# Kernel tuning notes

Hardware: AMD Instinct MI355X
Metric: run time of the kernel (lower is better)

The kernel has to match this reference:

```python
import jax, jax.numpy as jnp
import numpy as np

# dims
N = 50000      # total nodes in merged batch graph
M = 250000     # edges for GNN propagation
E = 200000     # candidate edges scored by mixture-Bernoulli head
MAXN = 512     # max_num_nodes (padded adjacency row length)
H = 128        # hidden_dim = embedding_dim = msg_dim
EF = 128       # edge_feat_dim = 2 * att_edge_dim
ATT = 128      # att_hidden_dim
K = 20         # num_mix_component
L = 3          # num_GNN_layers
S = 512        # num_subgraph
B = 16         # batch of graphs
C = 1          # num_canonical_order


def setup_inputs() -> dict:
    key = jax.random.key(0)
    ks = list(jax.random.split(key, 64))
    it = iter(ks)
    nk = lambda: next(it)
    d = {}
    d['node_feat'] = jax.random.normal(nk(), (N, MAXN), jnp.float32)
    d['edge'] = jax.random.randint(nk(), (M, 2), 0, N, dtype=jnp.int32)
    d['edge_feat'] = jax.random.normal(nk(), (M, EF), jnp.float32)
    d['node_idx_gnn'] = jax.random.randint(nk(), (E, 2), 0, N, dtype=jnp.int32)
    d['label'] = (jax.random.uniform(nk(), (E,)) < 0.1).astype(jnp.float32)
    # even sorted partition of E candidate edges into S subgraphs (all nonempty)
    d['subgraph_idx'] = ((jnp.arange(E) * S) // E).astype(jnp.int32)
    # bc_idx = repeat_interleave(arange(B*C), subgraphs_per_graph)
    d['bc_idx'] = jnp.repeat(jnp.arange(B * C, dtype=jnp.int32), S // (B * C))
    # params
    def lin(k, out_d, in_d):
        return jax.random.normal(k, (out_d, in_d), jnp.float32) * (1.0 / np.sqrt(in_d))
    d['dec_W'] = lin(nk(), H, MAXN); d['dec_b'] = jnp.zeros((H,), jnp.float32)
    d['msg_W1'] = jnp.stack([lin(nk(), H, H + EF) for _ in range(L)])
    d['msg_b1'] = jnp.zeros((L, H), jnp.float32)
    d['msg_W2'] = jnp.stack([lin(nk(), H, H) for _ in range(L)])
    d['msg_b2'] = jnp.zeros((L, H), jnp.float32)
    d['att_W1'] = jnp.stack([lin(nk(), ATT, H + EF) for _ in range(L)])
    d['att_b1'] = jnp.zeros((L, ATT), jnp.float32)
    d['att_W2'] = jnp.stack([lin(nk(), H, ATT) for _ in range(L)])
    d['att_b2'] = jnp.zeros((L, H), jnp.float32)
    d['gru_Wih'] = jnp.stack([lin(nk(), 3 * H, H) for _ in range(L)])
    d['gru_bih'] = jnp.zeros((L, 3 * H), jnp.float32)
    d['gru_Whh'] = jnp.stack([lin(nk(), 3 * H, H) for _ in range(L)])
    d['gru_bhh'] = jnp.zeros((L, 3 * H), jnp.float32)
    d['th_W1'] = lin(nk(), H, H); d['th_b1'] = jnp.zeros((H,), jnp.float32)
    d['th_W2'] = lin(nk(), H, H); d['th_b2'] = jnp.zeros((H,), jnp.float32)
    d['th_W3'] = lin(nk(), K, H); d['th_b3'] = jnp.zeros((K,), jnp.float32)
    d['al_W1'] = lin(nk(), H, H); d['al_b1'] = jnp.zeros((H,), jnp.float32)
    d['al_W2'] = lin(nk(), H, H); d['al_b2'] = jnp.zeros((H,), jnp.float32)
    d['al_W3'] = lin(nk(), K, H); d['al_b3'] = jnp.zeros((K,), jnp.float32)
    return d


def _gran_forward(node_feat, edge_feat, label, dec_W, dec_b, msg_W1, msg_b1,
                  msg_W2, msg_b2, att_W1, att_b1, att_W2, att_b2, gru_Wih,
                  gru_bih, gru_Whh, gru_bhh, th_W1, th_b1, th_W2, th_b2,
                  th_W3, th_b3, al_W1, al_b1, al_W2, al_b2, al_W3, al_b3,
                  edge, node_idx_gnn, subgraph_idx, bc_idx):
    n = node_feat.shape[0]
    # decoder_input: Linear(max_num_nodes -> embedding_dim)
    state = node_feat @ dec_W.T + dec_b  # [N, H]
    src, dst = edge[:, 0], edge[:, 1]
    for l in range(L):
        if l > 0:
            state = jax.nn.relu(state)
        # _prop: gather diff, msg MLP, sigmoid attention gate, scatter-sum, GRU
        diff = state[src] - state[dst]                       # [M, H]
        ei = jnp.concatenate([diff, edge_feat], axis=1)      # [M, H+EF]
        msg = jax.nn.relu(ei @ msg_W1[l].T + msg_b1[l]) @ msg_W2[l].T + msg_b2[l]
        att = jax.nn.sigmoid(jax.nn.relu(ei @ att_W1[l].T + att_b1[l]) @ att_W2[l].T + att_b2[l])
        agg = jax.ops.segment_sum(msg * att, dst, num_segments=n)  # [N, H]
        # torch GRUCell
        gi = agg @ gru_Wih[l].T + gru_bih[l]
        gh = state @ gru_Whh[l].T + gru_bhh[l]
        i_r, i_z, i_n = jnp.split(gi, 3, axis=-1)
        h_r, h_z, h_n = jnp.split(gh, 3, axis=-1)
        r = jax.nn.sigmoid(i_r + h_r)
        z = jax.nn.sigmoid(i_z + h_z)
        nn_ = jnp.tanh(i_n + r * h_n)
        state = (1.0 - z) * nn_ + z * state
    # mixture-Bernoulli heads on candidate-edge node-state diffs
    d2 = state[node_idx_gnn[:, 0]] - state[node_idx_gnn[:, 1]]  # [E, H]
    def mlp3(x, W1, b1, W2, b2, W3, b3):
        h = jax.nn.relu(x @ W1.T + b1)
        h = jax.nn.relu(h @ W2.T + b2)
        return h @ W3.T + b3
    log_theta = mlp3(d2, th_W1, th_b1, th_W2, th_b2, th_W3, th_b3)  # [E, K]
    log_alpha = mlp3(d2, al_W1, al_b1, al_W2, al_b2, al_W3, al_b3)  # [E, K]
    # mixture_bernoulli_loss (pos_weight = 1.0)
    y = label[:, None]
    adj_loss = jax.nn.softplus(-log_theta) + (1.0 - y) * log_theta  # BCEWithLogits, [E, K]
    const = jax.ops.segment_sum(jnp.ones((label.shape[0],), log_theta.dtype), subgraph_idx, num_segments=S)
    reduce_adj = jax.ops.segment_sum(adj_loss, subgraph_idx, num_segments=S)     # [S, K]
    reduce_la = jax.ops.segment_sum(log_alpha, subgraph_idx, num_segments=S)
    reduce_la = jax.nn.log_softmax(reduce_la / const[:, None], axis=-1)
    log_prob = jax.scipy.special.logsumexp(-reduce_adj + reduce_la, axis=1)      # [S]
    bc_log_prob = jax.ops.segment_sum(log_prob, bc_idx, num_segments=B * C)
    bc_const = jax.ops.segment_sum(const, bc_idx, num_segments=B * C)
    bc_loss = (bc_log_prob / bc_const).reshape(B, C)
    b_loss = jax.scipy.special.logsumexp(bc_loss, axis=1)  # logsumexp over orderings
    return jnp.mean(-b_loss)


def reference(node_feat, edge, edge_feat, node_idx_gnn, label, subgraph_idx,
              bc_idx, dec_W, dec_b, msg_W1, msg_b1, msg_W2, msg_b2, att_W1,
              att_b1, att_W2, att_b2, gru_Wih, gru_bih, gru_Whh, gru_bhh,
              th_W1, th_b1, th_W2, th_b2, th_W3, th_b3, al_W1, al_b1, al_W2,
              al_b2, al_W3, al_b3):
    return _gran_forward(node_feat, edge_feat, label, dec_W, dec_b, msg_W1,
                         msg_b1, msg_W2, msg_b2, att_W1, att_b1, att_W2,
                         att_b2, gru_Wih, gru_bih, gru_Whh, gru_bhh, th_W1,
                         th_b1, th_W2, th_b2, th_W3, th_b3, al_W1, al_b1,
                         al_W2, al_b2, al_W3, al_b3, edge, node_idx_gnn,
                         subgraph_idx, bc_idx)
```

## Files before the change

kernel.cpp:

```cpp
#include <hip/hip_runtime.h>
#include <cstdint>
#include <cstddef>


typedef __bf16 bf16x8 __attribute__((ext_vector_type(8)));
typedef short  s16x8  __attribute__((ext_vector_type(8)));
typedef short  s16x4  __attribute__((ext_vector_type(4)));
typedef float  f32x4  __attribute__((ext_vector_type(4)));

__device__ inline unsigned short f2bf(float f) {
    return __builtin_bit_cast(unsigned short, (__bf16)f);
}
__device__ inline float bf2f(unsigned short b) {
    return __uint_as_float(((unsigned int)b) << 16);
}
__device__ inline unsigned int pk2(float a, float b) {
    return ((unsigned int)f2bf(b) << 16) | f2bf(a);
}
__device__ inline f32x4 MFMA(bf16x8 a, bf16x8 b, f32x4 c) {
    return __builtin_amdgcn_mfma_f32_16x16x32_bf16(a, b, c, 0, 0, 0);
}

__device__ inline bf16x8 ld_swz(const char* lds, int row, int unit) {
    return *(const bf16x8*)(lds + row * 256 + ((unit ^ (row & 7)) << 4));
}
__device__ inline void hid_write(char* HID, int h0, int erow, s16x4 s4) {
    int unit = h0 >> 3;
    *(s16x4*)(HID + erow * 256 + ((unit ^ (erow & 7)) << 4) + ((h0 & 4) << 1)) = s4;
}
__device__ inline s16x4 ld_swz4(const char* lds, int row, int c0) {
    int unit = c0 >> 3;
    return *(const s16x4*)(lds + row * 256 + ((unit ^ (row & 7)) << 4) + ((c0 & 4) << 1));
}
__device__ inline bf16x8 ldA(const short* __restrict__ Wb, int K, int row, int koff) {
    return *(const bf16x8*)(Wb + (size_t)row * K + koff);
}
__device__ inline bf16x8 ld_f32_frag(const float* __restrict__ p) {
    float4 a = *(const float4*)p, b = *(const float4*)(p + 4);
    s16x8 s;
    s[0] = f2bf(a.x); s[1] = f2bf(a.y); s[2] = f2bf(a.z); s[3] = f2bf(a.w);
    s[4] = f2bf(b.x); s[5] = f2bf(b.y); s[6] = f2bf(b.z); s[7] = f2bf(b.w);
    return __builtin_bit_cast(bf16x8, s);
}

#define NPACK 31
struct PrepackArgs {
    const float* src[NPACK];
    short*       dst[NPACK];
    int stride[NPACK];
    int rows[NPACK];
    int rowsTot[NPACK];
    int cols[NPACK];
};

__global__ void prepack(PrepackArgs a) {
    int e = blockIdx.y;
    int row = blockIdx.x;
    if (row >= a.rowsTot[e]) return;
    int c8 = threadIdx.x;
    if (c8 * 8 >= a.cols[e]) return;
    s16x8 s = {};
    if (row < a.rows[e]) {
        const float* p = a.src[e] + (size_t)row * a.stride[e] + c8 * 8;
        float4 x = *(const float4*)p, y = *(const float4*)(p + 4);
        s[0] = f2bf(x.x); s[1] = f2bf(x.y); s[2] = f2bf(x.z); s[3] = f2bf(x.w);
        s[4] = f2bf(y.x); s[5] = f2bf(y.y); s[6] = f2bf(y.z); s[7] = f2bf(y.w);
    }
    *(s16x8*)(a.dst[e] + (size_t)row * a.cols[e] + c8 * 8) = s;
}

__device__ inline void proj_gemm_store(const char* ST, char* PJ,
                                       const short* __restrict__ projW,
                                       short* __restrict__ proj,
                                       int rb, int R, int tid)
{
    const int l = tid & 63, w = tid >> 6;
    f32x4 accP[2][2][4] = {};
#pragma unroll
    for (int ks = 0; ks < 4; ++ks) {
        int koff = ks * 32 + (l >> 4) * 8;
        bf16x8 aw[2][2];
#pragma unroll
        for (int pc = 0; pc < 2; ++pc)
#pragma unroll
            for (int mt = 0; mt < 2; ++mt)
                aw[pc][mt] = ldA(projW, 128, pc * 128 + 32 * w + 16 * mt + (l & 15), koff);
#pragma unroll
        for (int n = 0; n < 4; ++n) {
            bf16x8 b = ld_swz(ST, 16 * n + (l & 15), ks * 4 + (l >> 4));
#pragma unroll
            for (int pc = 0; pc < 2; ++pc)
#pragma unroll
                for (int mt = 0; mt < 2; ++mt)
                    accP[pc][mt][n] = MFMA(aw[pc][mt], b, accP[pc][mt][n]);
        }
    }
    const int half = w >> 1;
#pragma unroll
    for (int hh = 0; hh < 2; ++hh) {
        __syncthreads();
        if (half == hh) {
#pragma unroll
            for (int pc = 0; pc < 2; ++pc)
#pragma unroll
                for (int mt = 0; mt < 2; ++mt) {
                    int h0 = 32 * w + 16 * mt + ((l >> 4) << 2);
                    int colp = 2 * h0 + 4 * pc - 128 * hh;
#pragma unroll
                    for (int n = 0; n < 4; ++n) {
                        f32x4 v = accP[pc][mt][n];
                        s16x4 s4;
                        s4[0] = f2bf(v[0]); s4[1] = f2bf(v[1]);
                        s4[2] = f2bf(v[2]); s4[3] = f2bf(v[3]);
                        hid_write(PJ, colp, 16 * n + (l & 15), s4);
                    }
                }
        }
        __syncthreads();
#pragma unroll
        for (int p2 = 0; p2 < 4; ++p2) {
            int row = p2 * 16 + (tid >> 4);
            int r = rb + row;
            if (r < R) {
                bf16x8 v = ld_swz(PJ, row, tid & 15);
                *(s16x8*)(proj + (size_t)r * 256 + hh * 128 + (tid & 15) * 8) =
                    __builtin_bit_cast(s16x8, v);
            }
        }
    }
}

__global__ __launch_bounds__(256, 3)
void dec_proj(const float* __restrict__ nf, int R,
              const short* __restrict__ decWb, const float* __restrict__ bias,
              const short* __restrict__ projW,
              short* __restrict__ sOut, short* __restrict__ proj)
{
    __shared__ char ST[16384];
    __shared__ char PJ[16384];
    const int tid = threadIdx.x, l = tid & 63, w = tid >> 6;
    const int rb = blockIdx.x * 64;

    const float* brow[4];
#pragma unroll
    for (int n = 0; n < 4; ++n) {
        int row = rb + 16 * n + (l & 15); if (row >= R) row = R - 1;
        brow[n] = nf + (size_t)row * 512;
    }

    f32x4 acc[2][4] = {};
    for (int kc = 0; kc < 512; kc += 128) {
#pragma unroll
        for (int ks = 0; ks < 4; ++ks) {
            int koff = kc + ks * 32 + (l >> 4) * 8;
            bf16x8 a0 = ldA(decWb, 512, 32 * w + (l & 15), koff);
            bf16x8 a1 = ldA(decWb, 512, 32 * w + 16 + (l & 15), koff);
#pragma unroll
            for (int n = 0; n < 4; ++n) {
                bf16x8 b = ld_f32_frag(brow[n] + koff);
                acc[0][n] = MFMA(a0, b, acc[0][n]);
                acc[1][n] = MFMA(a1, b, acc[1][n]);
            }
        }
    }
#pragma unroll
    for (int mt = 0; mt < 2; ++mt) {
        int c0 = 32 * w + 16 * mt + ((l >> 4) << 2);
        float4 bv = *(const float4*)&bias[c0];
#pragma unroll
        for (int n = 0; n < 4; ++n) {
            f32x4 v = acc[mt][n];
            s16x4 s4;
            s4[0] = f2bf(v[0] + bv.x); s4[1] = f2bf(v[1] + bv.y);
            s4[2] = f2bf(v[2] + bv.z); s4[3] = f2bf(v[3] + bv.w);
            hid_write(ST, c0, 16 * n + (l & 15), s4);
        }
    }
    __syncthreads();
#pragma unroll
    for (int p2 = 0; p2 < 4; ++p2) {
        int row = p2 * 16 + (tid >> 4);
        int r = rb + row;
        if (r < R) {
            bf16x8 v = ld_swz(ST, row, tid & 15);
            *(s16x8*)(sOut + (size_t)r * 128 + (tid & 15) * 8) =
                __builtin_bit_cast(s16x8, v);
        }
    }
    proj_gemm_store(ST, PJ, projW, proj, rb, R, tid);
}

template<int HAS_PROJ>
__global__ __launch_bounds__(256, 2)
void node_fused4(const short* __restrict__ msgatt, const int* __restrict__ rowptr,
                 const short* __restrict__ sin_,
                 const short* __restrict__ Wih, const short* __restrict__ Whh,
                 const float* __restrict__ bih, const float* __restrict__ bhh,
                 const short* __restrict__ projW,
                 short* __restrict__ sOut, short* __restrict__ proj, int R)
{
    __shared__ char AGT[16384];
    __shared__ char SIN[16384];
    __shared__ char ST[16384];
    __shared__ char PJ[16384];
    const int tid = threadIdx.x, l = tid & 63, w = tid >> 6;
    const int rb = blockIdx.x * 64;

#pragma unroll 1
    for (int pass = 0; pass < 4; ++pass) {
        int row = pass * 16 + (tid >> 4);
        int node = rb + row;
        int u = tid & 15;
        float acc[8] = {};
        s16x8 sv = {};
        if (node < R) {
            int b = rowptr[node], e = rowptr[node + 1];
            for (int i = b; i < e; ++i) {
                s16x8 x = *(const s16x8*)(msgatt + (size_t)i * 128 + u * 8);
#pragma unroll
                for (int j = 0; j < 8; ++j) acc[j] += bf2f((unsigned short)x[j]);
            }
            sv = *(const s16x8*)(sin_ + (size_t)node * 128 + u * 8);
        }
        s16x8 o;
#pragma unroll
        for (int j = 0; j < 8; ++j) o[j] = f2bf(acc[j]);
        *(s16x8*)(AGT + row * 256 + ((u ^ (row & 7)) << 4)) = o;
        *(s16x8*)(SIN + row * 256 + ((u ^ (row & 7)) << 4)) = sv;
    }
    __syncthreads();

#pragma unroll 1
    for (int nh = 0; nh < 2; ++nh) {
        unsigned int rpk[2][2][2], zpk[2][2][2];
#pragma unroll 1
        for (int p = 0; p < 3; ++p) {
            f32x4 gia[2][2] = {}, gha[2][2] = {};
#pragma unroll
            for (int ks = 0; ks < 4; ++ks) {
                int koff = ks * 32 + (l >> 4) * 8;
                bf16x8 ai0 = ldA(Wih, 128, p * 128 + 32 * w + (l & 15), koff);
                bf16x8 ai1 = ldA(Wih, 128, p * 128 + 32 * w + 16 + (l & 15), koff);
                bf16x8 ah0 = ldA(Whh, 128, p * 128 + 32 * w + (l & 15), koff);
                bf16x8 ah1 = ldA(Whh, 128, p * 128 + 32 * w + 16 + (l & 15), koff);
#pragma unroll
                for (int n = 0; n < 2; ++n) {
                    int row = 32 * nh + 16 * n + (l & 15);
                    bf16x8 ba = ld_swz(AGT, row, ks * 4 + (l >> 4));
                    bf16x8 bs = ld_swz(SIN, row, ks * 4 + (l >> 4));
                    gia[0][n] = MFMA(ai0, ba, gia[0][n]);
                    gia[1][n] = MFMA(ai1, ba, gia[1][n]);
                    gha[0][n] = MFMA(ah0, bs, gha[0][n]);
                    gha[1][n] = MFMA(ah1, bs, gha[1][n]);
                }
            }
#pragma unroll
            for (int mt = 0; mt < 2; ++mt) {
                int c0 = 32 * w + 16 * mt + ((l >> 4) << 2);
                float4 bi = *(const float4*)&bih[p * 128 + c0];
                float4 bh = *(const float4*)&bhh[p * 128 + c0];
                float biv[4] = {bi.x, bi.y, bi.z, bi.w};
                float bhv[4] = {bh.x, bh.y, bh.z, bh.w};
#pragma unroll
                for (int n = 0; n < 2; ++n) {
                    int row = 32 * nh + 16 * n + (l & 15);
                    float gv[4], hv[4];
#pragma unroll
                    for (int q = 0; q < 4; ++q) {
                        gv[q] = gia[mt][n][q] + biv[q];
                        hv[q] = gha[mt][n][q] + bhv[q];
                    }
                    if (p == 0) {
                        rpk[mt][n][0] = pk2(1.f / (1.f + expf(-(gv[0] + hv[0]))),
                                            1.f / (1.f + expf(-(gv[1] + hv[1]))));
                        rpk[mt][n][1] = pk2(1.f / (1.f + expf(-(gv[2] + hv[2]))),
                                            1.f / (1.f + expf(-(gv[3] + hv[3]))));
                    } else if (p == 1) {
                        zpk[mt][n][0] = pk2(1.f / (1.f + expf(-(gv[0] + hv[0]))),
                                            1.f / (1.f + expf(-(gv[1] + hv[1]))));
                        zpk[mt][n][1] = pk2(1.f / (1.f + expf(-(gv[2] + hv[2]))),
                                            1.f / (1.f + expf(-(gv[3] + hv[3]))));
                    } else {
                        s16x4 sv = ld_swz4(SIN, row, c0);
                        s16x4 s4;
#pragma unroll
                        for (int q = 0; q < 4; ++q) {
                            unsigned int ru = rpk[mt][n][q >> 1], zu = zpk[mt][n][q >> 1];
                            float r = bf2f((unsigned short)((q & 1) ? (ru >> 16) : (ru & 0xffffu)));
                            float z = bf2f((unsigned short)((q & 1) ? (zu >> 16) : (zu & 0xffffu)));
                            float nn = tanhf(gv[q] + r * hv[q]);
                            float o = (1.f - z) * nn + z * bf2f((unsigned short)sv[q]);
                            s4[q] = f2bf(HAS_PROJ ? fmaxf(o, 0.f) : o);
                        }
                        hid_write(ST, c0, row, s4);
                    }
                }
            }
        }
    }
    __syncthreads();
#pragma unroll
    for (int p2 = 0; p2 < 4; ++p2) {
        int row = p2 * 16 + (tid >> 4);
        int r = rb + row;
        if (r < R) {
            bf16x8 v = ld_swz(ST, row, tid & 15);
            *(s16x8*)(sOut + (size_t)r * 128 + (tid & 15) * 8) =
                __builtin_bit_cast(s16x8, v);
        }
    }
    if (HAS_PROJ)
        proj_gemm_store(ST, PJ, projW, proj, rb, R, tid);
}

__global__ __launch_bounds__(256, 3)
void edge_fused2(const short* __restrict__ efc,
                 const int* __restrict__ srcs, const int* __restrict__ dsts,
                 const short* __restrict__ proj,
                 const short* __restrict__ mW1b, const short* __restrict__ mW2,
                 const short* __restrict__ aW1b, const short* __restrict__ aW2,
                 const float* __restrict__ mb1, const float* __restrict__ mb2,
                 const float* __restrict__ ab1, const float* __restrict__ ab2,
                 short* __restrict__ msgatt, int M, int ntiles)
{
    __shared__ char HIDm[16384];
    __shared__ char HIDa[16384];
    const int tid = threadIdx.x, l = tid & 63, w = tid >> 6;
    int q = ntiles >> 3, r = ntiles & 7;
    int xcd = blockIdx.x & 7, o = blockIdx.x >> 3;
    int tile = (xcd < r ? xcd * (q + 1) : r * (q + 1) + (xcd - r) * q) + o;
    const int pb = tile * 64;

    const char* erow[4];
    int dstv[4];
    s16x8 psv[2][4];
    {
#pragma unroll
        for (int n = 0; n < 4; ++n) {
            int pos = pb + 16 * n + (l & 15); if (pos >= M) pos = M - 1;
            int sv = srcs[pos];
            dstv[n] = dsts[pos];
            erow[n] = (const char*)(efc + (size_t)pos * 128);
#pragma unroll
            for (int mt = 0; mt < 2; ++mt) {
                int off = 2 * (32 * w + 16 * mt + ((l >> 4) << 2));
                psv[mt][n] = *(const s16x8*)(proj + (size_t)sv * 256 + off);
            }
        }
    }

    f32x4 accm[2][4] = {}, acca[2][4] = {};
#pragma unroll
    for (int ks = 0; ks < 4; ++ks) {
        int koff = ks * 32 + (l >> 4) * 8;
        bf16x8 am0 = ldA(mW1b, 128, 32 * w + (l & 15), koff);
        bf16x8 am1 = ldA(mW1b, 128, 32 * w + 16 + (l & 15), koff);
        bf16x8 aa0 = ldA(aW1b, 128, 32 * w + (l & 15), koff);
        bf16x8 aa1 = ldA(aW1b, 128, 32 * w + 16 + (l & 15), koff);
#pragma unroll
        for (int n = 0; n < 4; ++n) {
            bf16x8 b = *(const bf16x8*)(erow[n] + koff * 2);
            accm[0][n] = MFMA(am0, b, accm[0][n]);
            accm[1][n] = MFMA(am1, b, accm[1][n]);
            acca[0][n] = MFMA(aa0, b, acca[0][n]);
            acca[1][n] = MFMA(aa1, b, acca[1][n]);
        }
    }
#pragma unroll
    for (int mt = 0; mt < 2; ++mt) {
        int h0 = 32 * w + 16 * mt + ((l >> 4) << 2);
        float4 bm = *(const float4*)&mb1[h0];
        float4 ba = *(const float4*)&ab1[h0];
        float bmv[4] = {bm.x, bm.y, bm.z, bm.w};
        float bav[4] = {ba.x, ba.y, ba.z, ba.w};
#pragma unroll
        for (int n = 0; n < 4; ++n) {
            s16x8 ps = psv[mt][n];
            s16x8 pd = *(const s16x8*)(proj + (size_t)dstv[n] * 256 + 2 * h0);
            f32x4 vm = accm[mt][n], va = acca[mt][n];
            s16x4 sm, sa;
#pragma unroll
            for (int qq = 0; qq < 4; ++qq) {
                float m_ = vm[qq] + bmv[qq] + bf2f((unsigned short)ps[qq])
                           - bf2f((unsigned short)pd[qq]);
                float a_ = va[qq] + bav[qq] + bf2f((unsigned short)ps[qq + 4])
                           - bf2f((unsigned short)pd[qq + 4]);
                sm[qq] = f2bf(fmaxf(m_, 0.f));
                sa[qq] = f2bf(fmaxf(a_, 0.f));
            }
            hid_write(HIDm, h0, 16 * n + (l & 15), sm);
            hid_write(HIDa, h0, 16 * n + (l & 15), sa);
        }
    }
    __syncthreads();

    f32x4 acc2m[2][4] = {}, acc2a[2][4] = {};
#pragma unroll
    for (int ks = 0; ks < 4; ++ks) {
        int koff = ks * 32 + (l >> 4) * 8;
        bf16x8 wm0 = ldA(mW2, 128, 32 * w + (l & 15), koff);
        bf16x8 wm1 = ldA(mW2, 128, 32 * w + 16 + (l & 15), koff);
        bf16x8 wa0 = ldA(aW2, 128, 32 * w + (l & 15), koff);
        bf16x8 wa1 = ldA(aW2, 128, 32 * w + 16 + (l & 15), koff);
#pragma unroll
        for (int n = 0; n < 4; ++n) {
            bf16x8 bm = ld_swz(HIDm, 16 * n + (l & 15), ks * 4 + (l >> 4));
            bf16x8 ba = ld_swz(HIDa, 16 * n + (l & 15), ks * 4 + (l >> 4));
            acc2m[0][n] = MFMA(wm0, bm, acc2m[0][n]);
            acc2m[1][n] = MFMA(wm1, bm, acc2m[1][n]);
            acc2a[0][n] = MFMA(wa0, ba, acc2a[0][n]);
            acc2a[1][n] = MFMA(wa1, ba, acc2a[1][n]);
        }
    }
    __syncthreads();
#pragma unroll
    for (int mt = 0; mt < 2; ++mt) {
        int c0 = 32 * w + 16 * mt + ((l >> 4) << 2);
        float4 bm2 = *(const float4*)&mb2[c0];
        float4 ba2 = *(const float4*)&ab2[c0];
#pragma unroll
        for (int n = 0; n < 4; ++n) {
            f32x4 m_ = acc2m[mt][n], a_ = acc2a[mt][n];
            float o0 = (m_[0] + bm2.x) / (1.f + expf(-(a_[0] + ba2.x)));
            float o1 = (m_[1] + bm2.y) / (1.f + expf(-(a_[1] + ba2.y)));
            float o2 = (m_[2] + bm2.z) / (1.f + expf(-(a_[2] + ba2.z)));
            float o3 = (m_[3] + bm2.w) / (1.f + expf(-(a_[3] + ba2.w)));
            s16x4 s4;
            s4[0] = f2bf(o0); s4[1] = f2bf(o1); s4[2] = f2bf(o2); s4[3] = f2bf(o3);
            hid_write(HIDm, c0, 16 * n + (l & 15), s4);
        }
    }
    __syncthreads();
#pragma unroll
    for (int p2 = 0; p2 < 4; ++p2) {
        int row = p2 * 16 + (tid >> 4);
        int pos = pb + row;
        if (pos < M) {
            bf16x8 v = ld_swz(HIDm, row, tid & 15);
            *(s16x8*)(msgatt + (size_t)pos * 128 + (tid & 15) * 8) =
                __builtin_bit_cast(s16x8, v);
        }
    }
}

__global__ __launch_bounds__(256, 4)
void mlp_loss(const short* __restrict__ sP, const int* __restrict__ gidx,
              const float* __restrict__ label, const int* __restrict__ sg,
              const short* __restrict__ thW1, const short* __restrict__ thW2,
              const short* __restrict__ thW3,
              const float* __restrict__ thb1, const float* __restrict__ thb2,
              const float* __restrict__ thb3,
              const short* __restrict__ alW1, const short* __restrict__ alW2,
              const short* __restrict__ alW3,
              const float* __restrict__ alb1, const float* __restrict__ alb2,
              const float* __restrict__ alb3,
              float* __restrict__ radj, float* __restrict__ rla,
              float* __restrict__ cntS, int E, int S)
{
    __shared__ char D2T[16384];
    __shared__ char HID[16384];
    __shared__ float sacc[2][2][20];
    __shared__ float scnt[2];
    __shared__ int sbase;
    const int tid = threadIdx.x, l = tid & 63, w = tid >> 6;
    const int eb = blockIdx.x * 64;

    if (tid == 0) sbase = sg[eb];
    if (tid < 80) sacc[tid / 40][(tid / 20) & 1][tid % 20] = 0.f;

    if (w == 0) {
        int e = eb + l;
        bool valid = e < E;
        int lsv = valid ? sg[e] - sg[eb] : -1;
        unsigned long long m0 = __ballot(lsv == 0);
        unsigned long long m1 = __ballot(lsv == 1);
        if (l == 0) { scnt[0] = (float)__popcll(m0); scnt[1] = (float)__popcll(m1); }
    }

    for (int i = tid; i < 64 * 16; i += 256) {
        int row = i >> 4, u = i & 15;
        int e = eb + row; if (e >= E) e = E - 1;
        int2 ab = *(const int2*)&gidx[2 * (size_t)e];
        s16x8 x = *(const s16x8*)(sP + (size_t)ab.x * 128 + u * 8);
        s16x8 y = *(const s16x8*)(sP + (size_t)ab.y * 128 + u * 8);
        s16x8 d;
#pragma unroll
        for (int j = 0; j < 8; ++j)
            d[j] = f2bf(bf2f((unsigned short)x[j]) - bf2f((unsigned short)y[j]));
        *(s16x8*)(D2T + row * 256 + ((u ^ (row & 7)) << 4)) = d;
    }
    __syncthreads();

    for (int pass = 0; pass < 2; ++pass) {
        const short* W1 = pass ? alW1 : thW1;
        const short* W2 = pass ? alW2 : thW2;
        const short* W3 = pass ? alW3 : thW3;
        const float* b1 = pass ? alb1 : thb1;
        const float* b2 = pass ? alb2 : thb2;
        const float* b3 = pass ? alb3 : thb3;

        f32x4 acc[2][4] = {};
#pragma unroll
        for (int ks = 0; ks < 4; ++ks) {
            int koff = ks * 32 + (l >> 4) * 8;
            bf16x8 a0 = ldA(W1, 128, 32 * w + (l & 15), koff);
            bf16x8 a1 = ldA(W1, 128, 32 * w + 16 + (l & 15), koff);
#pragma unroll
            for (int n = 0; n < 4; ++n) {
                bf16x8 b = ld_swz(D2T, 16 * n + (l & 15), ks * 4 + (l >> 4));
                acc[0][n] = MFMA(a0, b, acc[0][n]);
                acc[1][n] = MFMA(a1, b, acc[1][n]);
            }
        }
        __syncthreads();
#pragma unroll
        for (int mt = 0; mt < 2; ++mt) {
            int h0 = 32 * w + 16 * mt + ((l >> 4) << 2);
            float4 bv = *(const float4*)&b1[h0];
#pragma unroll
            for (int n = 0; n < 4; ++n) {
                f32x4 v = acc[mt][n];
                s16x4 s4;
                s4[0] = f2bf(fmaxf(v[0] + bv.x, 0.f));
                s4[1] = f2bf(fmaxf(v[1] + bv.y, 0.f));
                s4[2] = f2bf(fmaxf(v[2] + bv.z, 0.f));
                s4[3] = f2bf(fmaxf(v[3] + bv.w, 0.f));
                hid_write(HID, h0, 16 * n + (l & 15), s4);
            }
        }
        __syncthreads();
        f32x4 acc2[2][4] = {};
#pragma unroll
        for (int ks = 0; ks < 4; ++ks) {
            int koff = ks * 32 + (l >> 4) * 8;
            bf16x8 a0 = ldA(W2, 128, 32 * w + (l & 15), koff);
            bf16x8 a1 = ldA(W2, 128, 32 * w + 16 + (l & 15), koff);
#pragma unroll
            for (int n = 0; n < 4; ++n) {
                bf16x8 b = ld_swz(HID, 16 * n + (l & 15), ks * 4 + (l >> 4));
                acc2[0][n] = MFMA(a0, b, acc2[0][n]);
                acc2[1][n] = MFMA(a1, b, acc2[1][n]);
            }
        }
        __syncthreads();
#pragma unroll
        for (int mt = 0; mt < 2; ++mt) {
            int h0 = 32 * w + 16 * mt + ((l >> 4) << 2);
            float4 bv = *(const float4*)&b2[h0];
#pragma unroll
            for (int n = 0; n < 4; ++n) {
                f32x4 v = acc2[mt][n];
                s16x4 s4;
                s4[0] = f2bf(fmaxf(v[0] + bv.x, 0.f));
                s4[1] = f2bf(fmaxf(v[1] + bv.y, 0.f));
                s4[2] = f2bf(fmaxf(v[2] + bv.z, 0.f));
                s4[3] = f2bf(fmaxf(v[3] + bv.w, 0.f));
                hid_write(HID, h0, 16 * n + (l & 15), s4);
            }
        }
        __syncthreads();
        f32x4 acc3[2] = {};
#pragma unroll
        for (int ks = 0; ks < 4; ++ks) {
            int koff = ks * 32 + (l >> 4) * 8;
            bf16x8 a0 = ldA(W3, 128, (l & 15), koff);
            bf16x8 a1 = ldA(W3, 128, 16 + (l & 15), koff);
            bf16x8 b = ld_swz(HID, 16 * w + (l & 15), ks * 4 + (l >> 4));
            acc3[0] = MFMA(a0, b, acc3[0]);
            acc3[1] = MFMA(a1, b, acc3[1]);
        }
        {
            int e = eb + 16 * w + (l & 15);
            bool val = e < E;
            float lsf = val ? (float)(sg[e] - sbase) : 0.f;
            float yv = (pass == 0 && val) ? label[e] : 0.f;
#pragma unroll
            for (int mt = 0; mt < 2; ++mt) {
#pragma unroll
                for (int qq = 0; qq < 4; ++qq) {
                    int k = 16 * mt + ((l >> 4) << 2) + qq;
                    bool kok = k < 20;
                    float bk = kok ? b3[k] : 0.f;
                    float vv = 0.f;
                    if (val && kok) {
                        float t = acc3[mt][qq] + bk;
                        if (pass == 0) {
                            float sp = fmaxf(-t, 0.f) + log1pf(expf(-fabsf(t)));
                            vv = sp + (1.f - yv) * t;
                        } else {
                            vv = t;
                        }
                    }
                    float vA = vv * (1.f - lsf), vB = vv * lsf;
                    vA += __shfl_xor(vA, 1); vB += __shfl_xor(vB, 1);
                    vA += __shfl_xor(vA, 2); vB += __shfl_xor(vB, 2);
                    vA += __shfl_xor(vA, 4); vB += __shfl_xor(vB, 4);
                    vA += __shfl_xor(vA, 8); vB += __shfl_xor(vB, 8);
                    if ((l & 15) == 0 && kok) {
                        atomicAdd(&sacc[pass][0][k], vA);
                        if (vB != 0.f) atomicAdd(&sacc[pass][1][k], vB);
                    }
                }
            }
        }
    }
    __syncthreads();
    if (tid < 40) {
        int ls = tid / 20, k = tid % 20;
        int s = sbase + ls;
        if (s < S) {
            float v  = sacc[0][ls][k];
            float v2 = sacc[1][ls][k];
            if (v  != 0.f) atomicAdd(&radj[s * 20 + k], v);
            if (v2 != 0.f) atomicAdd(&rla[s * 20 + k], v2);
        }
    }
    if (tid < 2) {
        int s = sbase + tid;
        if (s < S && scnt[tid] != 0.f) atomicAdd(&cntS[s], scnt[tid]);
    }
}

__global__ void csr_count(const int* __restrict__ edge, int* __restrict__ cnt, int M) {
    int e = blockIdx.x * 256 + threadIdx.x;
    if (e < M) atomicAdd(&cnt[edge[2 * (size_t)e + 1]], 1);
}

__global__ void csr_scan(const int* __restrict__ cnt, int* __restrict__ rowptr,
                         int* __restrict__ wofs, int N)
{
    __shared__ int part[1024];
    int t = threadIdx.x;
    int chunk = (N + 1023) / 1024;
    int b0 = t * chunk, b1 = b0 + chunk; if (b1 > N) b1 = N; if (b0 > N) b0 = N;
    int s = 0;
    for (int i = b0; i < b1; ++i) s += cnt[i];
    part[t] = s;
    __syncthreads();
    for (int off = 1; off < 1024; off <<= 1) {
        int v = (t >= off) ? part[t - off] : 0;
        __syncthreads();
        part[t] += v;
        __syncthreads();
    }
    int run = (t ? part[t - 1] : 0);
    for (int i = b0; i < b1; ++i) { rowptr[i] = run; wofs[i] = run; run += cnt[i]; }
    if (t == 1023) rowptr[N] = run;
}

__global__ void csr_scatter2(const int* __restrict__ edge, int* __restrict__ wofs,
                             int* __restrict__ eidx, int* __restrict__ srcs,
                             int* __restrict__ dsts, int M)
{
    int e = blockIdx.x * 256 + threadIdx.x;
    if (e < M) {
        int2 sd = *(const int2*)&edge[2 * (size_t)e];
        int p = atomicAdd(&wofs[sd.y], 1);
        eidx[p] = e; srcs[p] = sd.x; dsts[p] = sd.y;
    }
}

__global__ void ef_gather(const float* __restrict__ ef, const int* __restrict__ eidx,
                          short* __restrict__ efc, int M)
{
    long i = (long)blockIdx.x * 256 + threadIdx.x;
    if (i >= (long)M * 16) return;
    int p = (int)(i >> 4), u = (int)(i & 15);
    int e = eidx[p];
    const float* sp = ef + (size_t)e * 128 + u * 8;
    float4 a = *(const float4*)sp, b = *(const float4*)(sp + 4);
    s16x8 s;
    s[0] = f2bf(a.x); s[1] = f2bf(a.y); s[2] = f2bf(a.z); s[3] = f2bf(a.w);
    s[4] = f2bf(b.x); s[5] = f2bf(b.y); s[6] = f2bf(b.z); s[7] = f2bf(b.w);
    *(s16x8*)(efc + (size_t)p * 128 + u * 8) = s;
}

__global__ void final_kernel(const float* __restrict__ radj, const float* __restrict__ rla,
                             const float* __restrict__ cnt, const int* __restrict__ bc_idx,
                             float* __restrict__ out)
{
    __shared__ float bcl[16], bcc[16];
    const int s = threadIdx.x;
    if (s < 16) { bcl[s] = 0.f; bcc[s] = 0.f; }
    __syncthreads();
    float c = cnt[s];
    float x[20];
    float mx = -1e30f;
#pragma unroll
    for (int k = 0; k < 20; ++k) { x[k] = rla[s * 20 + k] / c; mx = fmaxf(mx, x[k]); }
    float se = 0.f;
#pragma unroll
    for (int k = 0; k < 20; ++k) se += expf(x[k] - mx);
    float lse = mx + logf(se);
    float t[20];
    float m2 = -1e30f;
#pragma unroll
    for (int k = 0; k < 20; ++k) { t[k] = -radj[s * 20 + k] + x[k] - lse; m2 = fmaxf(m2, t[k]); }
    float s2 = 0.f;
#pragma unroll
    for (int k = 0; k < 20; ++k) s2 += expf(t[k] - m2);
    float lp = m2 + logf(s2);
    atomicAdd(&bcl[bc_idx[s]], lp);
    atomicAdd(&bcc[bc_idx[s]], c);
    __syncthreads();
    if (s == 0) {
        float a = 0.f;
        for (int b = 0; b < 16; ++b) a += bcl[b] / bcc[b];
        out[0] = -a / 16.f;
    }
}

extern "C" void kernel_launch(void* const* d_in, const int* in_sizes, int n_in,
                              void* d_out, int out_size, void* d_ws, size_t ws_size,
                              hipStream_t stream)
{
    const float* node_feat = (const float*)d_in[0];
    const int*   edge      = (const int*)  d_in[1];
    const float* edge_feat = (const float*)d_in[2];
    const int*   gnn_idx   = (const int*)  d_in[3];
    const float* label     = (const float*)d_in[4];
    const int*   sg_idx    = (const int*)  d_in[5];
    const int*   bc_idx    = (const int*)  d_in[6];
    const float* dec_W  = (const float*)d_in[7];
    const float* dec_b  = (const float*)d_in[8];
    const float* msg_W1 = (const float*)d_in[9];
    const float* msg_b1 = (const float*)d_in[10];
    const float* msg_W2 = (const float*)d_in[11];
    const float* msg_b2 = (const float*)d_in[12];
    const float* att_W1 = (const float*)d_in[13];
    const float* att_b1 = (const float*)d_in[14];
    const float* att_W2 = (const float*)d_in[15];
    const float* att_b2 = (const float*)d_in[16];
    const float* gru_Wih = (const float*)d_in[17];
    const float* gru_bih = (const float*)d_in[18];
    const float* gru_Whh = (const float*)d_in[19];
    const float* gru_bhh = (const float*)d_in[20];
    const float* th_W1 = (const float*)d_in[21];
    const float* th_b1 = (const float*)d_in[22];
    const float* th_W2 = (const float*)d_in[23];
    const float* th_b2 = (const float*)d_in[24];
    const float* th_W3 = (const float*)d_in[25];
    const float* th_b3 = (const float*)d_in[26];
    const float* al_W1 = (const float*)d_in[27];
    const float* al_b1 = (const float*)d_in[28];
    const float* al_W2 = (const float*)d_in[29];
    const float* al_b2 = (const float*)d_in[30];
    const float* al_W3 = (const float*)d_in[31];
    const float* al_b3 = (const float*)d_in[32];

    const int N = in_sizes[0] / 512;
    const int M = in_sizes[1] / 2;
    const int E = in_sizes[3] / 2;
    const int S = in_sizes[6];

    size_t off = 0;
    auto alloc = [&](size_t bytes) {
        char* p = (char*)d_ws + off;
        off += (bytes + 255) & ~(size_t)255;
        return p;
    };
    short* decWb  = (short*)alloc((size_t)128 * 512 * 2);
    short* projWb = (short*)alloc((size_t)3 * 256 * 128 * 2);
    short* mW1bB  = (short*)alloc((size_t)3 * 128 * 128 * 2);
    short* aW1bB  = (short*)alloc((size_t)3 * 128 * 128 * 2);
    short* mW2B   = (short*)alloc((size_t)3 * 128 * 128 * 2);
    short* aW2B   = (short*)alloc((size_t)3 * 128 * 128 * 2);
    short* gihB   = (short*)alloc((size_t)3 * 384 * 128 * 2);
    short* ghhB   = (short*)alloc((size_t)3 * 384 * 128 * 2);
    short* thW1B  = (short*)alloc((size_t)128 * 128 * 2);
    short* thW2B  = (short*)alloc((size_t)128 * 128 * 2);
    short* thW3B  = (short*)alloc((size_t)32 * 128 * 2);
    short* alW1B  = (short*)alloc((size_t)128 * 128 * 2);
    short* alW2B  = (short*)alloc((size_t)128 * 128 * 2);
    short* alW3B  = (short*)alloc((size_t)32 * 128 * 2);
    short* sA     = (short*)alloc((size_t)N * 128 * 2);
    short* sB     = (short*)alloc((size_t)N * 128 * 2);
    short* sP     = (short*)alloc((size_t)N * 128 * 2);
    short* efc    = (short*)alloc((size_t)M * 128 * 2);
    short* msgatt = (short*)alloc((size_t)M * 128 * 2);
    short* proj   = (short*)alloc((size_t)N * 256 * 2);
    int*   cntN   = (int*)  alloc((size_t)N * 4);
    int*   wofs   = (int*)  alloc((size_t)N * 4);
    int*   rowptr = (int*)  alloc((size_t)(N + 1) * 4);
    int*   eidx   = (int*)  alloc((size_t)M * 4);
    int*   srcs   = (int*)  alloc((size_t)M * 4);
    int*   dsts   = (int*)  alloc((size_t)M * 4);
    float* radj   = (float*)alloc((size_t)S * 20 * 4);
    float* rla    = (float*)alloc((size_t)S * 20 * 4);
    float* cntS   = (float*)alloc((size_t)S * 4);

    PrepackArgs pa;
    int ei = 0;
    auto add = [&](const float* s, short* d, int stride, int rows, int rowsTot, int cols) {
        pa.src[ei] = s; pa.dst[ei] = d; pa.stride[ei] = stride;
        pa.rows[ei] = rows; pa.rowsTot[ei] = rowsTot; pa.cols[ei] = cols; ++ei;
    };
    add(dec_W, decWb, 512, 128, 128, 512);
    for (int l = 0; l < 3; ++l) {
        add(msg_W1 + (size_t)l * 128 * 256,       projWb + (size_t)l * 256 * 128,          256, 128, 128, 128);
        add(att_W1 + (size_t)l * 128 * 256,       projWb + (size_t)l * 256 * 128 + 16384,  256, 128, 128, 128);
        add(msg_W1 + (size_t)l * 128 * 256 + 128, mW1bB + (size_t)l * 16384,               256, 128, 128, 128);
        add(att_W1 + (size_t)l * 128 * 256 + 128, aW1bB + (size_t)l * 16384,               256, 128, 128, 128);
        add(msg_W2 + (size_t)l * 16384,           mW2B + (size_t)l * 16384,                128, 128, 128, 128);
        add(att_W2 + (size_t)l * 16384,           aW2B + (size_t)l * 16384,                128, 128, 128, 128);
        add(gru_Wih + (size_t)l * 49152,          gihB + (size_t)l * 49152,                128, 384, 384, 128);
        add(gru_Whh + (size_t)l * 49152,          ghhB + (size_t)l * 49152,                128, 384, 384, 128);
    }
    add(th_W1, thW1B, 128, 128, 128, 128);
    add(th_W2, thW2B, 128, 128, 128, 128);
    add(th_W3, thW3B, 128, 20, 32, 128);
    add(al_W1, alW1B, 128, 128, 128, 128);
    add(al_W2, alW2B, 128, 128, 128, 128);
    add(al_W3, alW3B, 128, 20, 32, 128);

    const dim3 blk(256);
    const int gN64 = (N + 63) / 64;
    const int gE64 = (E + 63) / 64;
    const int gMt  = (M + 255) / 256;
    const int ntilesM = (M + 63) / 64;

    hipMemsetAsync(radj, 0, (size_t)(S * 20 * 2 + S) * 4, stream);
    hipMemsetAsync(cntN, 0, (size_t)N * 4, stream);

    prepack<<<dim3(384, NPACK), dim3(64), 0, stream>>>(pa);

    csr_count   <<<gMt, blk, 0, stream>>>(edge, cntN, M);
    csr_scan    <<<1, 1024, 0, stream>>>(cntN, rowptr, wofs, N);
    csr_scatter2<<<gMt, blk, 0, stream>>>(edge, wofs, eidx, srcs, dsts, M);
    ef_gather   <<<(int)(((long)M * 16 + 255) / 256), blk, 0, stream>>>(edge_feat, eidx, efc, M);

    dec_proj<<<gN64, blk, 0, stream>>>(node_feat, N, decWb, dec_b, projWb, sA, proj);

    short* bufs[2] = { sA, sB };
    for (int l = 0; l < 3; ++l) {
        short* sin  = bufs[l & 1];
        short* sout = (l == 2) ? sP : bufs[(l + 1) & 1];
        edge_fused2<<<ntilesM, blk, 0, stream>>>(efc, srcs, dsts, proj,
            mW1bB + (size_t)l * 16384, mW2B + (size_t)l * 16384,
            aW1bB + (size_t)l * 16384, aW2B + (size_t)l * 16384,
            msg_b1 + l * 128, msg_b2 + l * 128,
            att_b1 + l * 128, att_b2 + l * 128,
            msgatt, M, ntilesM);
        if (l < 2) {
            node_fused4<1><<<gN64, blk, 0, stream>>>(msgatt, rowptr, sin,
                gihB + (size_t)l * 49152, ghhB + (size_t)l * 49152,
                gru_bih + l * 384, gru_bhh + l * 384,
                projWb + (size_t)(l + 1) * 256 * 128, sout, proj, N);
        } else {
            node_fused4<0><<<gN64, blk, 0, stream>>>(msgatt, rowptr, sin,
                gihB + (size_t)l * 49152, ghhB + (size_t)l * 49152,
                gru_bih + l * 384, gru_bhh + l * 384,
                nullptr, sout, nullptr, N);
        }
    }

    mlp_loss<<<gE64, blk, 0, stream>>>(sP, gnn_idx, label, sg_idx,
        thW1B, thW2B, thW3B, th_b1, th_b2, th_b3,
        alW1B, alW2B, alW3B, al_b1, al_b2, al_b3,
        radj, rla, cntS, E, S);
    final_kernel<<<1, S, 0, stream>>>(radj, rla, cntS, bc_idx, (float*)d_out);
}
```

Baseline: 1.048 ms.

## Process two edge tiles per block, prefetching second tile's gathers during first

The edge kernel now handles a pair of 64-edge tiles per block. It issues the second tile's src/dst index loads and projected-feature gathers while the first tile's MLP stages are still running, so gather latency is hidden behind MFMA work. This halves the grid size and raises register pressure, which may lower occupancy under the 3-blocks launch bound. The mlp_loss pass loop is also marked not to unroll, likely to limit code size and registers.

```diff
diff --git a/kernel.cpp b/kernel.cpp
--- a/kernel.cpp
+++ b/kernel.cpp
@@ -314,131 +314,243 @@
 }
 
 __global__ __launch_bounds__(256, 3)
-void edge_fused2(const short* __restrict__ efc,
+void edge_fused5(const short* __restrict__ efc,
                  const int* __restrict__ srcs, const int* __restrict__ dsts,
                  const short* __restrict__ proj,
                  const short* __restrict__ mW1b, const short* __restrict__ mW2,
                  const short* __restrict__ aW1b, const short* __restrict__ aW2,
                  const float* __restrict__ mb1, const float* __restrict__ mb2,
                  const float* __restrict__ ab1, const float* __restrict__ ab2,
-                 short* __restrict__ msgatt, int M, int ntiles)
+                 short* __restrict__ msgatt, int M, int npairs)
 {
     __shared__ char HIDm[16384];
     __shared__ char HIDa[16384];
     const int tid = threadIdx.x, l = tid & 63, w = tid >> 6;
-    int q = ntiles >> 3, r = ntiles & 7;
+    int q = npairs >> 3, r = npairs & 7;
     int xcd = blockIdx.x & 7, o = blockIdx.x >> 3;
-    int tile = (xcd < r ? xcd * (q + 1) : r * (q + 1) + (xcd - r) * q) + o;
-    const int pb = tile * 64;
-
-    const char* erow[4];
-    int dstv[4];
-    s16x8 psv[2][4];
+    int pair = (xcd < r ? xcd * (q + 1) : r * (q + 1) + (xcd - r) * q) + o;
+    const int pb0 = pair * 128;
+    const int pb1 = pb0 + 64;
+
+    const char* erow0[4];
+    int dstv0[4];
+    s16x8 psv0[2][4];
+#pragma unroll
+    for (int n = 0; n < 4; ++n) {
+        int pos = pb0 + 16 * n + (l & 15); if (pos >= M) pos = M - 1;
+        int sv = srcs[pos];
+        dstv0[n] = dsts[pos];
+        erow0[n] = (const char*)(efc + (size_t)pos * 128);
+#pragma unroll
+        for (int mt = 0; mt < 2; ++mt) {
+            int off = 2 * (32 * w + 16 * mt + ((l >> 4) << 2));
+            psv0[mt][n] = *(const s16x8*)(proj + (size_t)sv * 256 + off);
+        }
+    }
+
     {
-#pragma unroll
-        for (int n = 0; n < 4; ++n) {
-            int pos = pb + 16 * n + (l & 15); if (pos >= M) pos = M - 1;
-            int sv = srcs[pos];
-            dstv[n] = dsts[pos];
-            erow[n] = (const char*)(efc + (size_t)pos * 128);
-#pragma unroll
-            for (int mt = 0; mt < 2; ++mt) {
-                int off = 2 * (32 * w + 16 * mt + ((l >> 4) << 2));
-                psv[mt][n] = *(const s16x8*)(proj + (size_t)sv * 256 + off);
-            }
-        }
-    }
-
-    f32x4 accm[2][4] = {}, acca[2][4] = {};
-#pragma unroll
-    for (int ks = 0; ks < 4; ++ks) {
-        int koff = ks * 32 + (l >> 4) * 8;
-        bf16x8 am0 = ldA(mW1b, 128, 32 * w + (l & 15), koff);
-        bf16x8 am1 = ldA(mW1b, 128, 32 * w + 16 + (l & 15), koff);
-        bf16x8 aa0 = ldA(aW1b, 128, 32 * w + (l & 15), koff);
-        bf16x8 aa1 = ldA(aW1b, 128, 32 * w + 16 + (l & 15), koff);
-#pragma unroll
-        for (int n = 0; n < 4; ++n) {
-            bf16x8 b = *(const bf16x8*)(erow[n] + koff * 2);
-            accm[0][n] = MFMA(am0, b, accm[0][n]);
-            accm[1][n] = MFMA(am1, b, accm[1][n]);
-            acca[0][n] = MFMA(aa0, b, acca[0][n]);
-            acca[1][n] = MFMA(aa1, b, acca[1][n]);
-        }
-    }
-#pragma unroll
-    for (int mt = 0; mt < 2; ++mt) {
-        int h0 = 32 * w + 16 * mt + ((l >> 4) << 2);
-        float4 bm = *(const float4*)&mb1[h0];
-        float4 ba = *(const float4*)&ab1[h0];
-        float bmv[4] = {bm.x, bm.y, bm.z, bm.w};
-        float bav[4] = {ba.x, ba.y, ba.z, ba.w};
-#pragma unroll
-        for (int n = 0; n < 4; ++n) {
-            s16x8 ps = psv[mt][n];
-            s16x8 pd = *(const s16x8*)(proj + (size_t)dstv[n] * 256 + 2 * h0);
-            f32x4 vm = accm[mt][n], va = acca[mt][n];
-            s16x4 sm, sa;
-#pragma unroll
-            for (int qq = 0; qq < 4; ++qq) {
-                float m_ = vm[qq] + bmv[qq] + bf2f((unsigned short)ps[qq])
-                           - bf2f((unsigned short)pd[qq]);
-                float a_ = va[qq] + bav[qq] + bf2f((unsigned short)ps[qq + 4])
-                           - bf2f((unsigned short)pd[qq + 4]);
-                sm[qq] = f2bf(fmaxf(m_, 0.f));
-                sa[qq] = f2bf(fmaxf(a_, 0.f));
-            }
-            hid_write(HIDm, h0, 16 * n + (l & 15), sm);
-            hid_write(HIDa, h0, 16 * n + (l & 15), sa);
+        f32x4 accm[2][4] = {}, acca[2][4] = {};
+#pragma unroll
+        for (int ks = 0; ks < 4; ++ks) {
+            int koff = ks * 32 + (l >> 4) * 8;
+            bf16x8 am0 = ldA(mW1b, 128, 32 * w + (l & 15), koff);
+            bf16x8 am1 = ldA(mW1b, 128, 32 * w + 16 + (l & 15), koff);
+            bf16x8 aa0 = ldA(aW1b, 128, 32 * w + (l & 15), koff);
+            bf16x8 aa1 = ldA(aW1b, 128, 32 * w + 16 + (l & 15), koff);
+#pragma unroll
+            for (int n = 0; n < 4; ++n) {
+                bf16x8 b = *(const bf16x8*)(erow0[n] + koff * 2);
+                accm[0][n] = MFMA(am0, b, accm[0][n]);
+                accm[1][n] = MFMA(am1, b, accm[1][n]);
+                acca[0][n] = MFMA(aa0, b, acca[0][n]);
+                acca[1][n] = MFMA(aa1, b, acca[1][n]);
+            }
+        }
+#pragma unroll
+        for (int mt = 0; mt < 2; ++mt) {
+            int h0 = 32 * w + 16 * mt + ((l >> 4) << 2);
+            float4 bm = *(const float4*)&mb1[h0];
+            float4 ba = *(const float4*)&ab1[h0];
+            float bmv[4] = {bm.x, bm.y, bm.z, bm.w};
+            float bav[4] = {ba.x, ba.y, ba.z, ba.w};
+#pragma unroll
+            for (int n = 0; n < 4; ++n) {
+                s16x8 ps = psv0[mt][n];
+                s16x8 pd = *(const s16x8*)(proj + (size_t)dstv0[n] * 256 + 2 * h0);
+                f32x4 vm = accm[mt][n], va = acca[mt][n];
+                s16x4 sm, sa;
+#pragma unroll
+                for (int qq = 0; qq < 4; ++qq) {
+                    float m_ = vm[qq] + bmv[qq] + bf2f((unsigned short)ps[qq])
+                               - bf2f((unsigned short)pd[qq]);
+                    float a_ = va[qq] + bav[qq] + bf2f((unsigned short)ps[qq + 4])
+                               - bf2f((unsigned short)pd[qq + 4]);
+                    sm[qq] = f2bf(fmaxf(m_, 0.f));
+                    sa[qq] = f2bf(fmaxf(a_, 0.f));
+                }
+                hid_write(HIDm, h0, 16 * n + (l & 15), sm);
+                hid_write(HIDa, h0, 16 * n + (l & 15), sa);
+            }
+        }
+    }
+    const char* erow1[4];
+    int dstv1[4];
+    s16x8 psv1[2][4];
+#pragma unroll
+    for (int n = 0; n < 4; ++n) {
+        int pos = pb1 + 16 * n + (l & 15); if (pos >= M) pos = M - 1;
+        int sv = srcs[pos];
+        dstv1[n] = dsts[pos];
+        erow1[n] = (const char*)(efc + (size_t)pos * 128);
+#pragma unroll
+        for (int mt = 0; mt < 2; ++mt) {
+            int off = 2 * (32 * w + 16 * mt + ((l >> 4) << 2));
+            psv1[mt][n] = *(const s16x8*)(proj + (size_t)sv * 256 + off);
         }
     }
     __syncthreads();
-
-    f32x4 acc2m[2][4] = {}, acc2a[2][4] = {};
-#pragma unroll
-    for (int ks = 0; ks < 4; ++ks) {
-        int koff = ks * 32 + (l >> 4) * 8;
-        bf16x8 wm0 = ldA(mW2, 128, 32 * w + (l & 15), koff);
-        bf16x8 wm1 = ldA(mW2, 128, 32 * w + 16 + (l & 15), koff);
-        bf16x8 wa0 = ldA(aW2, 128, 32 * w + (l & 15), koff);
-        bf16x8 wa1 = ldA(aW2, 128, 32 * w + 16 + (l & 15), koff);
-#pragma unroll
-        for (int n = 0; n < 4; ++n) {
-            bf16x8 bm = ld_swz(HIDm, 16 * n + (l & 15), ks * 4 + (l >> 4));
-            bf16x8 ba = ld_swz(HIDa, 16 * n + (l & 15), ks * 4 + (l >> 4));
-            acc2m[0][n] = MFMA(wm0, bm, acc2m[0][n]);
-            acc2m[1][n] = MFMA(wm1, bm, acc2m[1][n]);
-            acc2a[0][n] = MFMA(wa0, ba, acc2a[0][n]);
-            acc2a[1][n] = MFMA(wa1, ba, acc2a[1][n]);
+    {
+        f32x4 acc2m[2][4] = {}, acc2a[2][4] = {};
+#pragma unroll
+        for (int ks = 0; ks < 4; ++ks) {
+            int koff = ks * 32 + (l >> 4) * 8;
+            bf16x8 wm0 = ldA(mW2, 128, 32 * w + (l & 15), koff);
+            bf16x8 wm1 = ldA(mW2, 128, 32 * w + 16 + (l & 15), koff);
+            bf16x8 wa0 = ldA(aW2, 128, 32 * w + (l & 15), koff);
+            bf16x8 wa1 = ldA(aW2, 128, 32 * w + 16 + (l & 15), koff);
+#pragma unroll
+            for (int n = 0; n < 4; ++n) {
+                bf16x8 bm = ld_swz(HIDm, 16 * n + (l & 15), ks * 4 + (l >> 4));
+                bf16x8 ba = ld_swz(HIDa, 16 * n + (l & 15), ks * 4 + (l >> 4));
+                acc2m[0][n] = MFMA(wm0, bm, acc2m[0][n]);
+                acc2m[1][n] = MFMA(wm1, bm, acc2m[1][n]);
+                acc2a[0][n] = MFMA(wa0, ba, acc2a[0][n]);
+                acc2a[1][n] = MFMA(wa1, ba, acc2a[1][n]);
+            }
+        }
+        __syncthreads();
+#pragma unroll
+        for (int mt = 0; mt < 2; ++mt) {
+            int c0 = 32 * w + 16 * mt + ((l >> 4) << 2);
+            float4 bm2 = *(const float4*)&mb2[c0];
+            float4 ba2 = *(const float4*)&ab2[c0];
+#pragma unroll
+            for (int n = 0; n < 4; ++n) {
+                f32x4 m_ = acc2m[mt][n], a_ = acc2a[mt][n];
+                float o0 = (m_[0] + bm2.x) / (1.f + expf(-(a_[0] + ba2.x)));
+                float o1 = (m_[1] + bm2.y) / (1.f + expf(-(a_[1] + ba2.y)));
+                float o2 = (m_[2] + bm2.z) / (1.f + expf(-(a_[2] + ba2.z)));
+                float o3 = (m_[3] + bm2.w) / (1.f + expf(-(a_[3] + ba2.w)));
+                s16x4 s4;
+                s4[0] = f2bf(o0); s4[1] = f2bf(o1); s4[2] = f2bf(o2); s4[3] = f2bf(o3);
+                hid_write(HIDm, c0, 16 * n + (l & 15), s4);
+            }
+        }
+        __syncthreads();
+#pragma unroll
+        for (int p2 = 0; p2 < 4; ++p2) {
+            int row = p2 * 16 + (tid >> 4);
+            int pos = pb0 + row;
+            if (pos < M) {
+                bf16x8 v = ld_swz(HIDm, row, tid & 15);
+                *(s16x8*)(msgatt + (size_t)pos * 128 + (tid & 15) * 8) =
+                    __builtin_bit_cast(s16x8, v);
+            }
         }
     }
     __syncthreads();
-#pragma unroll
-    for (int mt = 0; mt < 2; ++mt) {
-        int c0 = 32 * w + 16 * mt + ((l >> 4) << 2);
-        float4 bm2 = *(const float4*)&mb2[c0];
-        float4 ba2 = *(const float4*)&ab2[c0];
-#pragma unroll
-        for (int n = 0; n < 4; ++n) {
-            f32x4 m_ = acc2m[mt][n], a_ = acc2a[mt][n];
-            float o0 = (m_[0] + bm2.x) / (1.f + expf(-(a_[0] + ba2.x)));
-            float o1 = (m_[1] + bm2.y) / (1.f + expf(-(a_[1] + ba2.y)));
-            float o2 = (m_[2] + bm2.z) / (1.f + expf(-(a_[2] + ba2.z)));
-            float o3 = (m_[3] + bm2.w) / (1.f + expf(-(a_[3] + ba2.w)));
-            s16x4 s4;
-            s4[0] = f2bf(o0); s4[1] = f2bf(o1); s4[2] = f2bf(o2); s4[3] = f2bf(o3);
-            hid_write(HIDm, c0, 16 * n + (l & 15), s4);
-        }
-    }
-    __syncthreads();
-#pragma unroll
-    for (int p2 = 0; p2 < 4; ++p2) {
-        int row = p2 * 16 + (tid >> 4);
-        int pos = pb + row;
-        if (pos < M) {
-            bf16x8 v = ld_swz(HIDm, row, tid & 15);
-            *(s16x8*)(msgatt + (size_t)pos * 128 + (tid & 15) * 8) =
-                __builtin_bit_cast(s16x8, v);
+
+    if (pb1 < M) {
+        f32x4 accm[2][4] = {}, acca[2][4] = {};
+#pragma unroll
+        for (int ks = 0; ks < 4; ++ks) {
+            int koff = ks * 32 + (l >> 4) * 8;
+            bf16x8 am0 = ldA(mW1b, 128, 32 * w + (l & 15), koff);
+            bf16x8 am1 = ldA(mW1b, 128, 32 * w + 16 + (l & 15), koff);
+            bf16x8 aa0 = ldA(aW1b, 128, 32 * w + (l & 15), koff);
+            bf16x8 aa1 = ldA(aW1b, 128, 32 * w + 16 + (l & 15), koff);
+#pragma unroll
+            for (int n = 0; n < 4; ++n) {
+                bf16x8 b = *(const bf16x8*)(erow1[n] + koff * 2);
+                accm[0][n] = MFMA(am0, b, accm[0][n]);
+                accm[1][n] = MFMA(am1, b, accm[1][n]);
+                acca[0][n] = MFMA(aa0, b, acca[0][n]);
+                acca[1][n] = MFMA(aa1, b, acca[1][n]);
+            }
+        }
+#pragma unroll
+        for (int mt = 0; mt < 2; ++mt) {
+            int h0 = 32 * w + 16 * mt + ((l >> 4) << 2);
+            float4 bm = *(const float4*)&mb1[h0];
+            float4 ba = *(const float4*)&ab1[h0];
+            float bmv[4] = {bm.x, bm.y, bm.z, bm.w};
+            float bav[4] = {ba.x, ba.y, ba.z, ba.w};
+#pragma unroll
+            for (int n = 0; n < 4; ++n) {
+                s16x8 ps = psv1[mt][n];
+                s16x8 pd = *(const s16x8*)(proj + (size_t)dstv1[n] * 256 + 2 * h0);
+                f32x4 vm = accm[mt][n], va = acca[mt][n];
+                s16x4 sm, sa;
+#pragma unroll
+                for (int qq = 0; qq < 4; ++qq) {
+                    float m_ = vm[qq] + bmv[qq] + bf2f((unsigned short)ps[qq])
+                               - bf2f((unsigned short)pd[qq]);
+                    float a_ = va[qq] + bav[qq] + bf2f((unsigned short)ps[qq + 4])
+                               - bf2f((unsigned short)pd[qq + 4]);
+                    sm[qq] = f2bf(fmaxf(m_, 0.f));
+                    sa[qq] = f2bf(fmaxf(a_, 0.f));
+                }
+                hid_write(HIDm, h0, 16 * n + (l & 15), sm);
+                hid_write(HIDa, h0, 16 * n + (l & 15), sa);
+            }
+        }
+        __syncthreads();
+        f32x4 acc2m[2][4] = {}, acc2a[2][4] = {};
+#pragma unroll
+        for (int ks = 0; ks < 4; ++ks) {
+            int koff = ks * 32 + (l >> 4) * 8;
+            bf16x8 wm0 = ldA(mW2, 128, 32 * w + (l & 15), koff);
+            bf16x8 wm1 = ldA(mW2, 128, 32 * w + 16 + (l & 15), koff);
+            bf16x8 wa0 = ldA(aW2, 128, 32 * w + (l & 15), koff);
+            bf16x8 wa1 = ldA(aW2, 128, 32 * w + 16 + (l & 15), koff);
+#pragma unroll
+            for (int n = 0; n < 4; ++n) {
+                bf16x8 bm = ld_swz(HIDm, 16 * n + (l & 15), ks * 4 + (l >> 4));
+                bf16x8 ba = ld_swz(HIDa, 16 * n + (l & 15), ks * 4 + (l >> 4));
+                acc2m[0][n] = MFMA(wm0, bm, acc2m[0][n]);
+                acc2m[1][n] = MFMA(wm1, bm, acc2m[1][n]);
+                acc2a[0][n] = MFMA(wa0, ba, acc2a[0][n]);
+                acc2a[1][n] = MFMA(wa1, ba, acc2a[1][n]);
+            }
+        }
+        __syncthreads();
+#pragma unroll
+        for (int mt = 0; mt < 2; ++mt) {
+            int c0 = 32 * w + 16 * mt + ((l >> 4) << 2);
+            float4 bm2 = *(const float4*)&mb2[c0];
+            float4 ba2 = *(const float4*)&ab2[c0];
+#pragma unroll
+            for (int n = 0; n < 4; ++n) {
+                f32x4 m_ = acc2m[mt][n], a_ = acc2a[mt][n];
+                float o0 = (m_[0] + bm2.x) / (1.f + expf(-(a_[0] + ba2.x)));
+                float o1 = (m_[1] + bm2.y) / (1.f + expf(-(a_[1] + ba2.y)));
+                float o2 = (m_[2] + bm2.z) / (1.f + expf(-(a_[2] + ba2.z)));
+                float o3 = (m_[3] + bm2.w) / (1.f + expf(-(a_[3] + ba2.w)));
+                s16x4 s4;
+                s4[0] = f2bf(o0); s4[1] = f2bf(o1); s4[2] = f2bf(o2); s4[3] = f2bf(o3);
+                hid_write(HIDm, c0, 16 * n + (l & 15), s4);
+            }
+        }
+        __syncthreads();
+#pragma unroll
+        for (int p2 = 0; p2 < 4; ++p2) {
+            int row = p2 * 16 + (tid >> 4);
+            int pos = pb1 + row;
+            if (pos < M) {
+                bf16x8 v = ld_swz(HIDm, row, tid & 15);
+                *(s16x8*)(msgatt + (size_t)pos * 128 + (tid & 15) * 8) =
+                    __builtin_bit_cast(s16x8, v);
+            }
         }
     }
 }
@@ -491,6 +603,7 @@
     }
     __syncthreads();
 
+#pragma unroll 1
     for (int pass = 0; pass < 2; ++pass) {
         const short* W1 = pass ? alW1 : thW1;
         const short* W2 = pass ? alW2 : thW2;
@@ -818,6 +931,7 @@
     const int gE64 = (E + 63) / 64;
     const int gMt  = (M + 255) / 256;
     const int ntilesM = (M + 63) / 64;
+    const int npairs = (ntilesM + 1) / 2;
 
     hipMemsetAsync(radj, 0, (size_t)(S * 20 * 2 + S) * 4, stream);
     hipMemsetAsync(cntN, 0, (size_t)N * 4, stream);
@@ -835,12 +949,12 @@
     for (int l = 0; l < 3; ++l) {
         short* sin  = bufs[l & 1];
         short* sout = (l == 2) ? sP : bufs[(l + 1) & 1];
-        edge_fused2<<<ntilesM, blk, 0, stream>>>(efc, srcs, dsts, proj,
+        edge_fused5<<<npairs, blk, 0, stream>>>(efc, srcs, dsts, proj,
             mW1bB + (size_t)l * 16384, mW2B + (size_t)l * 16384,
             aW1bB + (size_t)l * 16384, aW2B + (size_t)l * 16384,
             msg_b1 + l * 128, msg_b2 + l * 128,
             att_b1 + l * 128, att_b2 + l * 128,
-            msgatt, M, ntilesM);
+            msgatt, M, npairs);
         if (l < 2) {
             node_fused4<1><<<gN64, blk, 0, stream>>>(msgatt, rowptr, sin,
                 gihB + (size_t)l * 49152, ghhB + (size_t)l * 49152,
```

After: 1.153 ms. 1.1x slower.
